# Kernel optimization log

Hardware: AMD Instinct MI355X
Metric: run time of the kernel (lower is better)

Reference implementation:

```python
import jax, jax.numpy as jnp
import numpy as np

B, R, D = 64, 4, 768
H = W = 37
ROI_SIDE = 5


def setup_inputs() -> dict:
    key = jax.random.key(0)
    k1, k2, k3 = jax.random.split(key, 3)
    return {
        "cls_tok": jax.random.normal(k1, (B, D), dtype=jnp.float32),
        "regs": jax.random.normal(k2, (B, R, D), dtype=jnp.float32),
        "patches2d": jax.random.normal(k3, (B, H, W, D), dtype=jnp.float32),
        "roi_side": ROI_SIDE,
    }


def reference(cls_tok, regs, patches2d, roi_side):
    # cues: [B, C, d] with C = 1 + n_registers
    cues = jnp.concatenate([cls_tok[:, None, :], regs], axis=1)
    b, h_dim, w_dim, d = patches2d.shape
    r = roi_side // 2

    # similarity of every cue against every patch: [B, C, H, W]
    sim = jnp.einsum('bcd,bhwd->bchw', cues, patches2d)
    idx = jnp.argmax(sim.reshape(b, cues.shape[1], h_dim * w_dim), axis=-1)  # [B, C]
    hh = idx // w_dim
    ww = idx % w_dim

    # clipped window slice [max(0,h-r), min(H,h+r+1)) == rows with |row-h| <= r
    rows = jnp.arange(h_dim)
    cols = jnp.arange(w_dim)
    rmask = jnp.abs(rows[None, None, :] - hh[:, :, None]) <= r  # [B, C, H]
    cmask = jnp.abs(cols[None, None, :] - ww[:, :, None]) <= r  # [B, C, W]
    mask = (rmask[:, :, :, None] & cmask[:, :, None, :]).astype(patches2d.dtype)  # [B,C,H,W]

    num = jnp.einsum('bchw,bhwd->bcd', mask, patches2d)
    cnt = jnp.sum(mask, axis=(2, 3))  # [B, C]
    rois = num / cnt[:, :, None]      # mean over the (clipped) ROI window

    toks = jnp.concatenate([cues, rois], axis=1)  # [B, 2C, d]
    nrm = jnp.maximum(jnp.linalg.norm(toks, axis=-1, keepdims=True), 1e-12)
    return toks / nrm
```

## Files before the change

### kernel.cpp

```cpp
#include <hip/hip_runtime.h>
#include <hip/hip_bf16.h>

#define NB   64
#define NREG 4
#define ND   768
#define NH   37
#define NW   37
#define NC   5
#define NP   (NH * NW)
#define BPB  16
#define PPB  ((NP + BPB - 1) / BPB)

__device__ __forceinline__ unsigned int ord_of(float f) {
    unsigned int u = __float_as_uint(f);
    return (u & 0x80000000u) ? ~u : (u | 0x80000000u);
}

__global__ __launch_bounds__(256, 4) void sim_argmax_kernel(
    const float* __restrict__ cls_tok,
    const float* __restrict__ regs,
    const float* __restrict__ patches,
    unsigned long long* __restrict__ pkeys)
{
    const int b    = blockIdx.x / BPB;
    const int pb   = blockIdx.x % BPB;
    const int wave = threadIdx.x >> 6;
    const int lane = threadIdx.x & 63;

    float4 cue[NC][3];
    #pragma unroll
    for (int c = 0; c < NC; ++c) {
        const float* cb = (c == 0) ? (cls_tok + (size_t)b * ND)
                                   : (regs + ((size_t)b * NREG + (c - 1)) * ND);
        #pragma unroll
        for (int k = 0; k < 3; ++k)
            cue[c][k] = *reinterpret_cast<const float4*>(cb + k * 256 + lane * 4);
    }

    float best[NC];
    int   bidx[NC];
    #pragma unroll
    for (int c = 0; c < NC; ++c) { best[c] = -3.4e38f; bidx[c] = 0; }

    const int pstart = pb * PPB;
    const int p1     = min(NP, pstart + PPB);

    int p = pstart + wave;
    if (p < p1) {
        const float* base = patches + ((size_t)b * NP + p) * ND + lane * 4;
        float4 v0 = *reinterpret_cast<const float4*>(base);
        float4 v1 = *reinterpret_cast<const float4*>(base + 256);
        float4 v2 = *reinterpret_cast<const float4*>(base + 512);

        while (true) {
            const int pn = p + 4;
            const bool more = pn < p1;
            float4 n0, n1, n2;
            if (more) {
                const float* nb = patches + ((size_t)b * NP + pn) * ND + lane * 4;
                n0 = *reinterpret_cast<const float4*>(nb);
                n1 = *reinterpret_cast<const float4*>(nb + 256);
                n2 = *reinterpret_cast<const float4*>(nb + 512);
            }

            float s[NC] = {0.f, 0.f, 0.f, 0.f, 0.f};
            #pragma unroll
            for (int c = 0; c < NC; ++c) {
                s[c] += v0.x * cue[c][0].x + v0.y * cue[c][0].y
                      + v0.z * cue[c][0].z + v0.w * cue[c][0].w;
                s[c] += v1.x * cue[c][1].x + v1.y * cue[c][1].y
                      + v1.z * cue[c][1].z + v1.w * cue[c][1].w;
                s[c] += v2.x * cue[c][2].x + v2.y * cue[c][2].y
                      + v2.z * cue[c][2].z + v2.w * cue[c][2].w;
            }
            #pragma unroll
            for (int c = 0; c < NC; ++c) {
                #pragma unroll
                for (int off = 32; off > 0; off >>= 1)
                    s[c] += __shfl_xor(s[c], off, 64);
                if (s[c] > best[c]) { best[c] = s[c]; bidx[c] = p; }
            }

            if (!more) break;
            v0 = n0; v1 = n1; v2 = n2; p = pn;
        }
    }

    __shared__ unsigned long long lk[4][NC];
    if (lane == 0) {
        #pragma unroll
        for (int c = 0; c < NC; ++c) {
            lk[wave][c] =
                ((unsigned long long)ord_of(best[c]) << 32) |
                (unsigned long long)(unsigned)(NP - 1 - bidx[c]);
        }
    }
    __syncthreads();
    if (threadIdx.x < NC) {
        unsigned long long k = lk[0][threadIdx.x];
        k = max(k, lk[1][threadIdx.x]);
        k = max(k, lk[2][threadIdx.x]);
        k = max(k, lk[3][threadIdx.x]);
        pkeys[(b * NC + threadIdx.x) * BPB + pb] = k;
    }
}

__global__ __launch_bounds__(256) void roi_norm_kernel(
    const float* __restrict__ cls_tok,
    const float* __restrict__ regs,
    const float* __restrict__ patches,
    const unsigned long long* __restrict__ pkeys,
    const int* __restrict__ roi_side_p,
    float* __restrict__ out)
{
    const int b   = blockIdx.x / NC;
    const int c   = blockIdx.x % NC;
    const int tid = threadIdx.x;
    const int wave = tid >> 6, lane = tid & 63;
    const int r = roi_side_p[0] >> 1;

    const unsigned long long* pk = pkeys + (b * NC + c) * BPB;
    unsigned long long key = pk[0];
    #pragma unroll
    for (int i = 1; i < BPB; ++i) key = max(key, pk[i]);

    const int idx = NP - 1 - (int)(key & 0xFFFFFFFFu);
    const int hh = idx / NW, ww = idx % NW;
    const int h0 = max(0, hh - r), h1 = min(NH - 1, hh + r);
    const int w0 = max(0, ww - r), w1 = min(NW - 1, ww + r);
    const float inv_cnt = 1.0f / (float)((h1 - h0 + 1) * (w1 - w0 + 1));

    float a0 = 0.f, a1 = 0.f, a2 = 0.f;
    for (int h = h0; h <= h1; ++h) {
        for (int w = w0; w <= w1; ++w) {
            const float* p = patches + ((size_t)b * NP + h * NW + w) * ND;
            a0 += p[tid];
            a1 += p[tid + 256];
            a2 += p[tid + 512];
        }
    }
    a0 *= inv_cnt; a1 *= inv_cnt; a2 *= inv_cnt;

    const float* cb = (c == 0) ? (cls_tok + (size_t)b * ND)
                               : (regs + ((size_t)b * NREG + (c - 1)) * ND);
    const float v0 = cb[tid], v1 = cb[tid + 256], v2 = cb[tid + 512];

    float sx = v0 * v0 + v1 * v1 + v2 * v2;
    float sy = a0 * a0 + a1 * a1 + a2 * a2;
    #pragma unroll
    for (int off = 32; off > 0; off >>= 1) {
        sx += __shfl_xor(sx, off, 64);
        sy += __shfl_xor(sy, off, 64);
    }
    __shared__ float red_x[4], red_y[4];
    if (lane == 0) { red_x[wave] = sx; red_y[wave] = sy; }
    __syncthreads();
    const float tot_x = red_x[0] + red_x[1] + red_x[2] + red_x[3];
    const float tot_y = red_y[0] + red_y[1] + red_y[2] + red_y[3];
    const float inv_nc = 1.0f / fmaxf(sqrtf(tot_x), 1e-12f);
    const float inv_nr = 1.0f / fmaxf(sqrtf(tot_y), 1e-12f);

    float* oc = out + ((size_t)b * 2 * NC + c) * ND;
    float* om = out + ((size_t)b * 2 * NC + NC + c) * ND;
    oc[tid]       = v0 * inv_nc;
    oc[tid + 256] = v1 * inv_nc;
    oc[tid + 512] = v2 * inv_nc;
    om[tid]       = a0 * inv_nr;
    om[tid + 256] = a1 * inv_nr;
    om[tid + 512] = a2 * inv_nr;
}

extern "C" void kernel_launch(void* const* d_in, const int* in_sizes, int n_in,
                              void* d_out, int out_size, void* d_ws, size_t ws_size,
                              hipStream_t stream) {
    const float* cls_tok = (const float*)d_in[0];
    const float* regs    = (const float*)d_in[1];
    const float* patches = (const float*)d_in[2];
    const int*   roi     = (const int*)d_in[3];
    float* out = (float*)d_out;
    unsigned long long* pkeys = (unsigned long long*)d_ws;

    sim_argmax_kernel<<<NB * BPB, 256, 0, stream>>>(cls_tok, regs, patches, pkeys);
    roi_norm_kernel<<<NB * NC, 256, 0, stream>>>(cls_tok, regs, patches, pkeys, roi, out);
}
```

Before: 59.36 us.

## Fuse argmax and ROI-normalize kernels using last-block-done atomic counter

Merges the similarity/argmax kernel and the ROI mean/normalize kernel into one launch. Each wave publishes its own partial argmax key, and a per-batch atomic counter picks the last finishing block to reduce the keys and compute all five ROI means and normalisations serially. This removes the second kernel launch and its dependency gap, but adds a memset launch. It also concentrates the ROI work on 64 blocks that each loop over 5 cues, which lowers the parallelism of that phase.

```diff
diff --git a/kernel.cpp b/kernel.cpp
--- a/kernel.cpp
+++ b/kernel.cpp
@@ -10,22 +10,28 @@
 #define NP   (NH * NW)
 #define BPB  16
 #define PPB  ((NP + BPB - 1) / BPB)
+#define NWAVE 4
+#define KEYS_PER_BC (BPB * NWAVE)
 
 __device__ __forceinline__ unsigned int ord_of(float f) {
     unsigned int u = __float_as_uint(f);
     return (u & 0x80000000u) ? ~u : (u | 0x80000000u);
 }
 
-__global__ __launch_bounds__(256, 4) void sim_argmax_kernel(
+__global__ __launch_bounds__(256, 4) void fused_encoder_kernel(
     const float* __restrict__ cls_tok,
     const float* __restrict__ regs,
     const float* __restrict__ patches,
-    unsigned long long* __restrict__ pkeys)
+    const int* __restrict__ roi_side_p,
+    float* __restrict__ out,
+    unsigned long long* __restrict__ pkeys,
+    unsigned int* __restrict__ cnt)
 {
     const int b    = blockIdx.x / BPB;
     const int pb   = blockIdx.x % BPB;
     const int wave = threadIdx.x >> 6;
     const int lane = threadIdx.x & 63;
+    const int tid  = threadIdx.x;
 
     float4 cue[NC][3];
     #pragma unroll
@@ -46,14 +52,14 @@
     const int p1     = min(NP, pstart + PPB);
 
     int p = pstart + wave;
-    if (p < p1) {
+    {
         const float* base = patches + ((size_t)b * NP + p) * ND + lane * 4;
         float4 v0 = *reinterpret_cast<const float4*>(base);
         float4 v1 = *reinterpret_cast<const float4*>(base + 256);
         float4 v2 = *reinterpret_cast<const float4*>(base + 512);
 
         while (true) {
-            const int pn = p + 4;
+            const int pn = p + NWAVE;
             const bool more = pn < p1;
             float4 n0, n1, n2;
             if (more) {
@@ -86,88 +92,94 @@
         }
     }
 
-    __shared__ unsigned long long lk[4][NC];
     if (lane == 0) {
         #pragma unroll
         for (int c = 0; c < NC; ++c) {
-            lk[wave][c] =
+            unsigned long long key =
                 ((unsigned long long)ord_of(best[c]) << 32) |
                 (unsigned long long)(unsigned)(NP - 1 - bidx[c]);
-        }
-    }
+            atomicExch(&pkeys[(size_t)(b * NC + c) * KEYS_PER_BC + pb * NWAVE + wave], key);
+        }
+    }
+
     __syncthreads();
-    if (threadIdx.x < NC) {
-        unsigned long long k = lk[0][threadIdx.x];
-        k = max(k, lk[1][threadIdx.x]);
-        k = max(k, lk[2][threadIdx.x]);
-        k = max(k, lk[3][threadIdx.x]);
-        pkeys[(b * NC + threadIdx.x) * BPB + pb] = k;
-    }
-}
-
-__global__ __launch_bounds__(256) void roi_norm_kernel(
-    const float* __restrict__ cls_tok,
-    const float* __restrict__ regs,
-    const float* __restrict__ patches,
-    const unsigned long long* __restrict__ pkeys,
-    const int* __restrict__ roi_side_p,
-    float* __restrict__ out)
-{
-    const int b   = blockIdx.x / NC;
-    const int c   = blockIdx.x % NC;
-    const int tid = threadIdx.x;
-    const int wave = tid >> 6, lane = tid & 63;
+    __shared__ int winner_flag;
+    if (tid == 0) {
+        __threadfence();
+        unsigned int old = atomicAdd(&cnt[b], 1u);
+        winner_flag = (old == BPB - 1) ? 1 : 0;
+    }
+    __syncthreads();
+    if (!winner_flag) return;
+
+    __threadfence();
+
+    __shared__ unsigned long long final_key[NC];
+    #pragma unroll
+    for (int c = 0; c < NC; ++c) {
+        if (wave == (c & 3) && (c < 4 || wave == 0)) {
+            unsigned long long k =
+                atomicAdd((unsigned long long*)&pkeys[(size_t)(b * NC + c) * KEYS_PER_BC + lane], 0ull);
+            #pragma unroll
+            for (int off = 32; off > 0; off >>= 1) {
+                unsigned long long o = __shfl_xor(k, off, 64);
+                k = max(k, o);
+            }
+            if (lane == 0) final_key[c] = k;
+        }
+    }
+    __syncthreads();
+
     const int r = roi_side_p[0] >> 1;
-
-    const unsigned long long* pk = pkeys + (b * NC + c) * BPB;
-    unsigned long long key = pk[0];
-    #pragma unroll
-    for (int i = 1; i < BPB; ++i) key = max(key, pk[i]);
-
-    const int idx = NP - 1 - (int)(key & 0xFFFFFFFFu);
-    const int hh = idx / NW, ww = idx % NW;
-    const int h0 = max(0, hh - r), h1 = min(NH - 1, hh + r);
-    const int w0 = max(0, ww - r), w1 = min(NW - 1, ww + r);
-    const float inv_cnt = 1.0f / (float)((h1 - h0 + 1) * (w1 - w0 + 1));
-
-    float a0 = 0.f, a1 = 0.f, a2 = 0.f;
-    for (int h = h0; h <= h1; ++h) {
-        for (int w = w0; w <= w1; ++w) {
-            const float* p = patches + ((size_t)b * NP + h * NW + w) * ND;
-            a0 += p[tid];
-            a1 += p[tid + 256];
-            a2 += p[tid + 512];
-        }
-    }
-    a0 *= inv_cnt; a1 *= inv_cnt; a2 *= inv_cnt;
-
-    const float* cb = (c == 0) ? (cls_tok + (size_t)b * ND)
-                               : (regs + ((size_t)b * NREG + (c - 1)) * ND);
-    const float v0 = cb[tid], v1 = cb[tid + 256], v2 = cb[tid + 512];
-
-    float sx = v0 * v0 + v1 * v1 + v2 * v2;
-    float sy = a0 * a0 + a1 * a1 + a2 * a2;
-    #pragma unroll
-    for (int off = 32; off > 0; off >>= 1) {
-        sx += __shfl_xor(sx, off, 64);
-        sy += __shfl_xor(sy, off, 64);
-    }
-    __shared__ float red_x[4], red_y[4];
-    if (lane == 0) { red_x[wave] = sx; red_y[wave] = sy; }
-    __syncthreads();
-    const float tot_x = red_x[0] + red_x[1] + red_x[2] + red_x[3];
-    const float tot_y = red_y[0] + red_y[1] + red_y[2] + red_y[3];
-    const float inv_nc = 1.0f / fmaxf(sqrtf(tot_x), 1e-12f);
-    const float inv_nr = 1.0f / fmaxf(sqrtf(tot_y), 1e-12f);
-
-    float* oc = out + ((size_t)b * 2 * NC + c) * ND;
-    float* om = out + ((size_t)b * 2 * NC + NC + c) * ND;
-    oc[tid]       = v0 * inv_nc;
-    oc[tid + 256] = v1 * inv_nc;
-    oc[tid + 512] = v2 * inv_nc;
-    om[tid]       = a0 * inv_nr;
-    om[tid + 256] = a1 * inv_nr;
-    om[tid + 512] = a2 * inv_nr;
+    __shared__ float red_x[NWAVE], red_y[NWAVE];
+
+    for (int c = 0; c < NC; ++c) {
+        const unsigned long long key = final_key[c];
+        const int idx = NP - 1 - (int)(key & 0xFFFFFFFFu);
+        const int hh = idx / NW, ww = idx % NW;
+        const int h0 = max(0, hh - r), h1 = min(NH - 1, hh + r);
+        const int w0 = max(0, ww - r), w1 = min(NW - 1, ww + r);
+        const float inv_cnt = 1.0f / (float)((h1 - h0 + 1) * (w1 - w0 + 1));
+
+        float a0 = 0.f, a1 = 0.f, a2 = 0.f;
+        for (int h = h0; h <= h1; ++h) {
+            for (int w = w0; w <= w1; ++w) {
+                const float* pp = patches + ((size_t)b * NP + h * NW + w) * ND;
+                a0 += pp[tid];
+                a1 += pp[tid + 256];
+                a2 += pp[tid + 512];
+            }
+        }
+        a0 *= inv_cnt; a1 *= inv_cnt; a2 *= inv_cnt;
+
+        const float* cb = (c == 0) ? (cls_tok + (size_t)b * ND)
+                                   : (regs + ((size_t)b * NREG + (c - 1)) * ND);
+        const float v0 = cb[tid], v1 = cb[tid + 256], v2 = cb[tid + 512];
+
+        float sx = v0 * v0 + v1 * v1 + v2 * v2;
+        float sy = a0 * a0 + a1 * a1 + a2 * a2;
+        #pragma unroll
+        for (int off = 32; off > 0; off >>= 1) {
+            sx += __shfl_xor(sx, off, 64);
+            sy += __shfl_xor(sy, off, 64);
+        }
+        if (lane == 0) { red_x[wave] = sx; red_y[wave] = sy; }
+        __syncthreads();
+        const float tot_x = red_x[0] + red_x[1] + red_x[2] + red_x[3];
+        const float tot_y = red_y[0] + red_y[1] + red_y[2] + red_y[3];
+        const float inv_nc = 1.0f / fmaxf(sqrtf(tot_x), 1e-12f);
+        const float inv_nr = 1.0f / fmaxf(sqrtf(tot_y), 1e-12f);
+
+        float* oc = out + ((size_t)b * 2 * NC + c) * ND;
+        float* om = out + ((size_t)b * 2 * NC + NC + c) * ND;
+        oc[tid]       = v0 * inv_nc;
+        oc[tid + 256] = v1 * inv_nc;
+        oc[tid + 512] = v2 * inv_nc;
+        om[tid]       = a0 * inv_nr;
+        om[tid + 256] = a1 * inv_nr;
+        om[tid + 512] = a2 * inv_nr;
+        __syncthreads();
+    }
 }
 
 extern "C" void kernel_launch(void* const* d_in, const int* in_sizes, int n_in,
@@ -178,8 +190,13 @@
     const float* patches = (const float*)d_in[2];
     const int*   roi     = (const int*)d_in[3];
     float* out = (float*)d_out;
+
     unsigned long long* pkeys = (unsigned long long*)d_ws;
-
-    sim_argmax_kernel<<<NB * BPB, 256, 0, stream>>>(cls_tok, regs, patches, pkeys);
-    roi_norm_kernel<<<NB * NC, 256, 0, stream>>>(cls_tok, regs, patches, pkeys, roi, out);
+    unsigned int* cnt = (unsigned int*)((char*)d_ws +
+                         (size_t)NB * NC * KEYS_PER_BC * sizeof(unsigned long long));
+
+    hipMemsetAsync(cnt, 0, NB * sizeof(unsigned int), stream);
+
+    fused_encoder_kernel<<<NB * BPB, 256, 0, stream>>>(
+        cls_tok, regs, patches, roi, out, pkeys, cnt);
 }
```

Result: slower. 143.8 us (+142.3%).

## Double-buffer patch prefetch two rows ahead and use DPP wave reduction

Applied to the files above, without the earlier changes.

The argmax kernel now keeps two register buffers of patch vectors (A/B) and prefetches two iterations ahead instead of one, aiming to hide more global-memory latency. The cross-lane reduction replaces the five shuffle-xor steps with a DPP row-shift/broadcast sequence that leaves the full sum in lane 63, so lane 63 now writes the per-wave keys. This cuts the LDS-backed shuffle traffic but uses more registers. It also assumes every wave has at least one patch (the first load is unguarded), which holds for the fixed sizes here.

```diff
diff --git a/kernel.cpp b/kernel.cpp
--- a/kernel.cpp
+++ b/kernel.cpp
@@ -10,10 +10,26 @@
 #define NP   (NH * NW)
 #define BPB  16
 #define PPB  ((NP + BPB - 1) / BPB)
+#define NWAVE 4
 
 __device__ __forceinline__ unsigned int ord_of(float f) {
     unsigned int u = __float_as_uint(f);
     return (u & 0x80000000u) ? ~u : (u | 0x80000000u);
+}
+
+template <int CTRL>
+__device__ __forceinline__ float dpp_add_step(float x) {
+    int y = __builtin_amdgcn_update_dpp(0, __float_as_int(x), CTRL, 0xf, 0xf, true);
+    return x + __int_as_float(y);
+}
+__device__ __forceinline__ float wave_sum_lane63(float x) {
+    x = dpp_add_step<0x111>(x);
+    x = dpp_add_step<0x112>(x);
+    x = dpp_add_step<0x114>(x);
+    x = dpp_add_step<0x118>(x);
+    x = dpp_add_step<0x142>(x);
+    x = dpp_add_step<0x143>(x);
+    return x;
 }
 
 __global__ __launch_bounds__(256, 4) void sim_argmax_kernel(
@@ -44,50 +60,83 @@
 
     const int pstart = pb * PPB;
     const int p1     = min(NP, pstart + PPB);
-
+    const size_t bb  = (size_t)b * NP;
+
+    float4 A0, A1, A2, B0, B1, B2;
     int p = pstart + wave;
-    if (p < p1) {
-        const float* base = patches + ((size_t)b * NP + p) * ND + lane * 4;
-        float4 v0 = *reinterpret_cast<const float4*>(base);
-        float4 v1 = *reinterpret_cast<const float4*>(base + 256);
-        float4 v2 = *reinterpret_cast<const float4*>(base + 512);
-
-        while (true) {
-            const int pn = p + 4;
-            const bool more = pn < p1;
-            float4 n0, n1, n2;
-            if (more) {
-                const float* nb = patches + ((size_t)b * NP + pn) * ND + lane * 4;
-                n0 = *reinterpret_cast<const float4*>(nb);
-                n1 = *reinterpret_cast<const float4*>(nb + 256);
-                n2 = *reinterpret_cast<const float4*>(nb + 512);
-            }
-
-            float s[NC] = {0.f, 0.f, 0.f, 0.f, 0.f};
-            #pragma unroll
-            for (int c = 0; c < NC; ++c) {
-                s[c] += v0.x * cue[c][0].x + v0.y * cue[c][0].y
-                      + v0.z * cue[c][0].z + v0.w * cue[c][0].w;
-                s[c] += v1.x * cue[c][1].x + v1.y * cue[c][1].y
-                      + v1.z * cue[c][1].z + v1.w * cue[c][1].w;
-                s[c] += v2.x * cue[c][2].x + v2.y * cue[c][2].y
-                      + v2.z * cue[c][2].z + v2.w * cue[c][2].w;
-            }
-            #pragma unroll
-            for (int c = 0; c < NC; ++c) {
-                #pragma unroll
-                for (int off = 32; off > 0; off >>= 1)
-                    s[c] += __shfl_xor(s[c], off, 64);
-                if (s[c] > best[c]) { best[c] = s[c]; bidx[c] = p; }
-            }
-
-            if (!more) break;
-            v0 = n0; v1 = n1; v2 = n2; p = pn;
-        }
-    }
-
-    __shared__ unsigned long long lk[4][NC];
-    if (lane == 0) {
+    {
+        const float* a = patches + (bb + p) * ND + lane * 4;
+        A0 = *reinterpret_cast<const float4*>(a);
+        A1 = *reinterpret_cast<const float4*>(a + 256);
+        A2 = *reinterpret_cast<const float4*>(a + 512);
+    }
+    if (p + NWAVE < p1) {
+        const float* q = patches + (bb + p + NWAVE) * ND + lane * 4;
+        B0 = *reinterpret_cast<const float4*>(q);
+        B1 = *reinterpret_cast<const float4*>(q + 256);
+        B2 = *reinterpret_cast<const float4*>(q + 512);
+    } else {
+        B0 = B1 = B2 = make_float4(0.f, 0.f, 0.f, 0.f);
+    }
+
+    while (true) {
+        {
+            float s[NC];
+            #pragma unroll
+            for (int c = 0; c < NC; ++c) {
+                s[c] = A0.x * cue[c][0].x + A0.y * cue[c][0].y
+                     + A0.z * cue[c][0].z + A0.w * cue[c][0].w
+                     + A1.x * cue[c][1].x + A1.y * cue[c][1].y
+                     + A1.z * cue[c][1].z + A1.w * cue[c][1].w
+                     + A2.x * cue[c][2].x + A2.y * cue[c][2].y
+                     + A2.z * cue[c][2].z + A2.w * cue[c][2].w;
+            }
+            const int pf = p + 2 * NWAVE;
+            if (pf < p1) {
+                const float* a = patches + (bb + pf) * ND + lane * 4;
+                A0 = *reinterpret_cast<const float4*>(a);
+                A1 = *reinterpret_cast<const float4*>(a + 256);
+                A2 = *reinterpret_cast<const float4*>(a + 512);
+            }
+            #pragma unroll
+            for (int c = 0; c < NC; ++c) {
+                float t = wave_sum_lane63(s[c]);
+                if (t > best[c]) { best[c] = t; bidx[c] = p; }
+            }
+        }
+        p += NWAVE;
+        if (p >= p1) break;
+
+        {
+            float s[NC];
+            #pragma unroll
+            for (int c = 0; c < NC; ++c) {
+                s[c] = B0.x * cue[c][0].x + B0.y * cue[c][0].y
+                     + B0.z * cue[c][0].z + B0.w * cue[c][0].w
+                     + B1.x * cue[c][1].x + B1.y * cue[c][1].y
+                     + B1.z * cue[c][1].z + B1.w * cue[c][1].w
+                     + B2.x * cue[c][2].x + B2.y * cue[c][2].y
+                     + B2.z * cue[c][2].z + B2.w * cue[c][2].w;
+            }
+            const int pf = p + 2 * NWAVE;
+            if (pf < p1) {
+                const float* q = patches + (bb + pf) * ND + lane * 4;
+                B0 = *reinterpret_cast<const float4*>(q);
+                B1 = *reinterpret_cast<const float4*>(q + 256);
+                B2 = *reinterpret_cast<const float4*>(q + 512);
+            }
+            #pragma unroll
+            for (int c = 0; c < NC; ++c) {
+                float t = wave_sum_lane63(s[c]);
+                if (t > best[c]) { best[c] = t; bidx[c] = p; }
+            }
+        }
+        p += NWAVE;
+        if (p >= p1) break;
+    }
+
+    __shared__ unsigned long long lk[NWAVE][NC];
+    if (lane == 63) {
         #pragma unroll
         for (int c = 0; c < NC; ++c) {
             lk[wave][c] =
```

Measured after the change: 57.17 us. 1.04x faster.

## Stage patches via async global-to-LDS loads and use DPP wave reductions

Applied to the files above, without the earlier changes.

Replaces the register double-buffered patch loads with direct global_load_lds DMA into a two-deep LDS ring per wave, synchronised with explicit vmcnt/lgkmcnt waits, so the next patch's fetch overlaps the dot products. It also replaces the shuffle-xor butterfly reductions with a DPP row/broadcast sequence that leaves each sum in lane 63, and moves the per-wave key write to lane 63. This adds LDS traffic and depends on hand-written waitcnt values being right. The kernel is memory-bound, so the gain mostly comes from cheaper reductions and better latency hiding.

```diff
diff --git a/kernel.cpp b/kernel.cpp
--- a/kernel.cpp
+++ b/kernel.cpp
@@ -10,10 +10,39 @@
 #define NP   (NH * NW)
 #define BPB  16
 #define PPB  ((NP + BPB - 1) / BPB)
+#define NWAVE 4
+#define DEPTH 2
 
 __device__ __forceinline__ unsigned int ord_of(float f) {
     unsigned int u = __float_as_uint(f);
     return (u & 0x80000000u) ? ~u : (u | 0x80000000u);
+}
+
+template <int CTRL>
+__device__ __forceinline__ float dpp_add_step(float x) {
+    int y = __builtin_amdgcn_update_dpp(0, __float_as_int(x), CTRL, 0xf, 0xf, true);
+    return x + __int_as_float(y);
+}
+__device__ __forceinline__ float wave_sum_lane63(float x) {
+    x = dpp_add_step<0x111>(x);
+    x = dpp_add_step<0x112>(x);
+    x = dpp_add_step<0x114>(x);
+    x = dpp_add_step<0x118>(x);
+    x = dpp_add_step<0x142>(x);
+    x = dpp_add_step<0x143>(x);
+    return x;
+}
+
+__device__ __forceinline__ void stage_patch(const float* __restrict__ gbase,
+                                            float* lslot, int lane) {
+    const float* g = gbase + lane * 4;
+    #pragma unroll
+    for (int k = 0; k < 3; ++k) {
+        __builtin_amdgcn_global_load_lds(
+            (const __attribute__((address_space(1))) void*)(g + k * 256),
+            (__attribute__((address_space(3))) void*)(lslot + k * 256),
+            16, 0, 0);
+    }
 }
 
 __global__ __launch_bounds__(256, 4) void sim_argmax_kernel(
@@ -27,6 +56,8 @@
     const int wave = threadIdx.x >> 6;
     const int lane = threadIdx.x & 63;
 
+    __shared__ float lds[DEPTH][NWAVE][ND];
+
     float4 cue[NC][3];
     #pragma unroll
     for (int c = 0; c < NC; ++c) {
@@ -44,50 +75,52 @@
 
     const int pstart = pb * PPB;
     const int p1     = min(NP, pstart + PPB);
-
-    int p = pstart + wave;
-    if (p < p1) {
-        const float* base = patches + ((size_t)b * NP + p) * ND + lane * 4;
-        float4 v0 = *reinterpret_cast<const float4*>(base);
-        float4 v1 = *reinterpret_cast<const float4*>(base + 256);
-        float4 v2 = *reinterpret_cast<const float4*>(base + 512);
-
-        while (true) {
-            const int pn = p + 4;
-            const bool more = pn < p1;
-            float4 n0, n1, n2;
-            if (more) {
-                const float* nb = patches + ((size_t)b * NP + pn) * ND + lane * 4;
-                n0 = *reinterpret_cast<const float4*>(nb);
-                n1 = *reinterpret_cast<const float4*>(nb + 256);
-                n2 = *reinterpret_cast<const float4*>(nb + 512);
-            }
-
-            float s[NC] = {0.f, 0.f, 0.f, 0.f, 0.f};
-            #pragma unroll
-            for (int c = 0; c < NC; ++c) {
-                s[c] += v0.x * cue[c][0].x + v0.y * cue[c][0].y
-                      + v0.z * cue[c][0].z + v0.w * cue[c][0].w;
-                s[c] += v1.x * cue[c][1].x + v1.y * cue[c][1].y
-                      + v1.z * cue[c][1].z + v1.w * cue[c][1].w;
-                s[c] += v2.x * cue[c][2].x + v2.y * cue[c][2].y
-                      + v2.z * cue[c][2].z + v2.w * cue[c][2].w;
-            }
-            #pragma unroll
-            for (int c = 0; c < NC; ++c) {
-                #pragma unroll
-                for (int off = 32; off > 0; off >>= 1)
-                    s[c] += __shfl_xor(s[c], off, 64);
-                if (s[c] > best[c]) { best[c] = s[c]; bidx[c] = p; }
-            }
-
-            if (!more) break;
-            v0 = n0; v1 = n1; v2 = n2; p = pn;
-        }
-    }
-
-    __shared__ unsigned long long lk[4][NC];
-    if (lane == 0) {
+    const size_t bb  = (size_t)b * NP;
+    const int p0     = pstart + wave;
+
+    #pragma unroll
+    for (int s = 0; s < DEPTH; ++s) {
+        const int pp = p0 + s * NWAVE;
+        if (pp < p1) stage_patch(patches + (bb + pp) * ND, &lds[s][wave][0], lane);
+    }
+
+    int it = 0;
+    for (int pp = p0; pp < p1; pp += NWAVE, ++it) {
+        const int s = it & 1;
+        const bool more = (pp + NWAVE) < p1;
+
+        if (more) asm volatile("s_waitcnt vmcnt(3)" ::: "memory");
+        else      asm volatile("s_waitcnt vmcnt(0)" ::: "memory");
+
+        const float* l = &lds[s][wave][0] + lane * 4;
+        const float4 v0 = *reinterpret_cast<const float4*>(l);
+        const float4 v1 = *reinterpret_cast<const float4*>(l + 256);
+        const float4 v2 = *reinterpret_cast<const float4*>(l + 512);
+
+        asm volatile("s_waitcnt lgkmcnt(0)" ::: "memory");
+
+        const int pf = pp + DEPTH * NWAVE;
+        if (pf < p1) stage_patch(patches + (bb + pf) * ND, &lds[s][wave][0], lane);
+
+        float sacc[NC];
+        #pragma unroll
+        for (int c = 0; c < NC; ++c) {
+            sacc[c] = v0.x * cue[c][0].x + v0.y * cue[c][0].y
+                    + v0.z * cue[c][0].z + v0.w * cue[c][0].w
+                    + v1.x * cue[c][1].x + v1.y * cue[c][1].y
+                    + v1.z * cue[c][1].z + v1.w * cue[c][1].w
+                    + v2.x * cue[c][2].x + v2.y * cue[c][2].y
+                    + v2.z * cue[c][2].z + v2.w * cue[c][2].w;
+        }
+        #pragma unroll
+        for (int c = 0; c < NC; ++c) {
+            const float t = wave_sum_lane63(sacc[c]);
+            if (t > best[c]) { best[c] = t; bidx[c] = pp; }
+        }
+    }
+
+    __shared__ unsigned long long lk[NWAVE][NC];
+    if (lane == 63) {
         #pragma unroll
         for (int c = 0; c < NC; ++c) {
             lk[wave][c] =
```

New measurement: 57.47 us. -3.2%, faster.
